# Kernel tuning notes

Measured on AMD Instinct MI355X. Metric: run time of the kernel, lower is better.

Reference implementation:

```python
import jax, jax.numpy as jnp
import numpy as np

N = 100000      # total nodes
E = 1600000     # total edges
B = 256         # graphs in batch
D_IN = 64       # node_in_dim
D_EMB = 128     # node_emb_dim
D_G = 128       # graph_emb_dim
L = 3           # gnn_layers
H1, H2 = 32, 8  # decoder MLP hidden dims
EPS_LN = 1e-5


def layernorm(h, g, b):
    mu = jnp.mean(h, -1, keepdims=True)
    var = jnp.mean((h - mu) ** 2, -1, keepdims=True)
    return (h - mu) * jax.lax.rsqrt(var + EPS_LN) * g + b


def setup_inputs() -> dict:
    key = jax.random.key(0)
    ks = jax.random.split(key, 16)
    gi = D_IN + D_EMB  # skip-conn GNN input dim

    def w(k, shape, fan):
        return jax.random.normal(k, shape, jnp.float32) / np.sqrt(fan).astype(np.float32)

    return {
        "x": jax.random.normal(ks[0], (N, D_IN), jnp.float32),
        "edge_index": jax.random.randint(ks[1], (2, E), 0, N),
        "batch_indices": jnp.sort(jax.random.randint(ks[2], (N,), 0, B)),
        "W_in": w(ks[3], (D_IN, D_EMB), D_IN), "b_in": jnp.zeros((D_EMB,), jnp.float32),
        "eps": jnp.zeros((L,), jnp.float32),  # GINConv train_eps init 0
        "mlp_W1": w(ks[4], (L, gi, D_EMB), gi), "mlp_b1": jnp.zeros((L, D_EMB), jnp.float32),
        "mlp_W2": w(ks[5], (L, D_EMB, D_EMB), D_EMB), "mlp_b2": jnp.zeros((L, D_EMB), jnp.float32),
        "ln_g": jnp.ones((L, D_EMB), jnp.float32), "ln_b": jnp.zeros((L, D_EMB), jnp.float32),
        "out_W": w(ks[6], (D_EMB, D_EMB), D_EMB), "out_b": jnp.zeros((D_EMB,), jnp.float32),
        "lnf_g": jnp.ones((D_EMB,), jnp.float32), "lnf_b": jnp.zeros((D_EMB,), jnp.float32),
        "graph_W": w(ks[7], (D_EMB, D_G), D_EMB), "graph_b": jnp.zeros((D_G,), jnp.float32),
        "gln_g": jnp.ones((D_G,), jnp.float32), "gln_b": jnp.zeros((D_G,), jnp.float32),
        "dW1": w(ks[8], (D_IN + D_EMB, H1), D_IN + D_EMB), "db1": jnp.zeros((H1,), jnp.float32),
        "dW2": w(ks[9], (H1, H2), H1), "db2": jnp.zeros((H2,), jnp.float32),
        "dW3": w(ks[10], (H2, 1), H2), "db3": jnp.zeros((1,), jnp.float32),
        "gW1": w(ks[11], (D_G, H1), D_G), "gb1": jnp.zeros((H1,), jnp.float32),
        "gW2": w(ks[12], (H1, H2), H1), "gb2": jnp.zeros((H2,), jnp.float32),
        "gW3": w(ks[13], (H2, 1), H2), "gb3": jnp.zeros((1,), jnp.float32),
    }


def reference(x, edge_index, batch_indices, W_in, b_in, eps, mlp_W1, mlp_b1, mlp_W2, mlp_b2,
              ln_g, ln_b, out_W, out_b, lnf_g, lnf_b, graph_W, graph_b, gln_g, gln_b,
              dW1, db1, dW2, db2, dW3, db3, gW1, gb1, gW2, gb2, gW3, gb3):
    src, dst = edge_index[0], edge_index[1]
    # Encoder: node_in_fc
    h = jax.nn.relu(x @ W_in + b_in)
    for l in range(L):
        gin = jnp.concatenate([x, h], -1)  # skip_conn: [N, D_IN+D_EMB]
        # GIN message passing: sum-aggregate neighbor features at target nodes
        agg = jax.ops.segment_sum(gin[src], dst, num_segments=N)
        z = (1.0 + eps[l]) * gin + agg
        z = jax.nn.relu(z @ mlp_W1[l] + mlp_b1[l]) @ mlp_W2[l] + mlp_b2[l]
        h = jax.nn.elu(layernorm(z, ln_g[l], ln_b[l]))
    # graph embedding: per-node fc+LN then global mean pool over batch segments
    ge = layernorm(jax.nn.relu(h @ graph_W + graph_b), gln_g, gln_b)
    sums = jax.ops.segment_sum(ge, batch_indices, num_segments=B)
    cnt = jax.ops.segment_sum(jnp.ones((N,), ge.dtype), batch_indices, num_segments=B)
    graph_emb = sums / jnp.maximum(cnt, 1.0)[:, None]
    # node_out_fc + final LN
    node_emb = layernorm(jax.nn.relu(h @ out_W + out_b), lnf_g, lnf_b)
    # Decoder: nodewise MLP on [x, node_emb] (skip_conn)
    ni = jnp.concatenate([x, node_emb], -1)
    no = jax.nn.relu(ni @ dW1 + db1)
    no = (jax.nn.relu(no @ dW2 + db2) @ dW3 + db3)[:, 0]  # [N]
    # graphwise residual MLP
    go = jax.nn.relu(graph_emb @ gW1 + gb1)
    go = (jax.nn.relu(go @ gW2 + gb2) @ gW3 + gb3)[:, 0]  # [B]
    return jnp.concatenate([no, go], -1)  # [N+B]
```

## Files before the change

kernel.cpp:

```cpp
#include <hip/hip_runtime.h>
#include <hip/hip_bf16.h>

#define D_IN 64
#define D_EMB 128
#define GI 192
#define H1 32
#define H2 8

typedef __attribute__((ext_vector_type(8))) short bf16x8;
typedef __attribute__((ext_vector_type(4))) float f32x4;

__device__ __forceinline__ unsigned short f2bf(float f) {
    unsigned int u = __float_as_uint(f);
    return (unsigned short)((u + 0x7fffu + ((u >> 16) & 1u)) >> 16);
}
__device__ __forceinline__ float bflo(unsigned int u) { return __uint_as_float(u << 16); }
__device__ __forceinline__ float bfhi(unsigned int u) { return __uint_as_float(u & 0xffff0000u); }
__device__ __forceinline__ unsigned int pk2(unsigned short a, unsigned short b) {
    return (unsigned int)a | ((unsigned int)b << 16);
}

__global__ __launch_bounds__(256) void hist_part_k(const int* __restrict__ dst, int* __restrict__ cnt,
                                                   int E, int N8) {
    int p = blockIdx.x & 7;
// ... 57 lines not shown
    }
}

__global__ __launch_bounds__(256) void scatter_part_k(const int* __restrict__ src, const int* __restrict__ dst,
                                                      int* __restrict__ cursor, int* __restrict__ csr,
                                                      int E, int N8) {
    int p = blockIdx.x & 7;
    int base = (blockIdx.x >> 3) * 1024;
    int lo = p * N8, hi = lo + N8;
    #pragma unroll
    for (int t = 0; t < 4; ++t) {
        int e = base + t * 256 + threadIdx.x;
        if (e < E) {
            int d = dst[e];
            if (d >= lo && d < hi) {
                int s = src[e];
                int pos = atomicAdd(&cursor[d], 1);
                csr[pos] = s;
            }
        }
    }
}

__global__ __launch_bounds__(256) void xcvt_k(const float* __restrict__ x, unsigned short* __restrict__ xb,
                                              int total4) {
    int i = blockIdx.x * 256 + threadIdx.x;
    if (i < total4) {
        float4 v = ((const float4*)x)[i];
        ((uint2*)xb)[i] = make_uint2(pk2(f2bf(v.x), f2bf(v.y)), pk2(f2bf(v.z), f2bf(v.w)));
    }
}

__global__ __launch_bounds__(256) void wfrag_all_k(
    const float* __restrict__ W_in, const float* __restrict__ mlp_W1, const float* __restrict__ mlp_W2,
    const float* __restrict__ graph_W, const float* __restrict__ out_W,
    unsigned short* __restrict__ wf_in, unsigned short* __restrict__ wf_w1,
    unsigned short* __restrict__ wf_w2, unsigned short* __restrict__ wf_graph,
    unsigned short* __restrict__ wf_out) {
    int idx = blockIdx.x * 256 + threadIdx.x;
    const float* src;
    unsigned short* dst;
    int local;
    if (idx < 8192) { src = W_in; dst = wf_in; local = idx; }
    else if (idx < 81920) { int t = idx - 8192; int l = t / 24576; local = t - l * 24576;
                            src = mlp_W1 + (size_t)l * 24576; dst = wf_w1 + (size_t)l * 24576; }
    else if (idx < 131072) { int t = idx - 81920; int l = t / 16384; local = t - l * 16384;
                             src = mlp_W2 + (size_t)l * 16384; dst = wf_w2 + (size_t)l * 16384; }
    else if (idx < 147456) { local = idx - 131072; src = graph_W; dst = wf_graph; }
    else { local = idx - 147456; src = out_W; dst = wf_out; }
    int k = local >> 7, c = local & 127;
    dst[(((size_t)(k >> 3) * 128) + c) * 8 + (k & 7)] = f2bf(src[local]);
}

__global__ __launch_bounds__(256) void agg64b_k(const unsigned short* __restrict__ xb,
                                                const int* __restrict__ rp, const int* __restrict__ cs,
                                                float* __restrict__ out, int N) {
    int n = blockIdx.x * 8 + (threadIdx.x >> 5);
    int lane = threadIdx.x & 31;
    if (n >= N) return;
    int bg = rp[n], e = rp[n + 1];
    const unsigned int* x2 = (const unsigned int*)xb;
    float sx = 0.f, sy = 0.f;
    int j = bg;
    for (; j + 3 < e; j += 4) {
        unsigned int v0 = x2[(size_t)cs[j] * 32 + lane];
        unsigned int v1 = x2[(size_t)cs[j + 1] * 32 + lane];
        unsigned int v2 = x2[(size_t)cs[j + 2] * 32 + lane];
        unsigned int v3 = x2[(size_t)cs[j + 3] * 32 + lane];
        sx += bflo(v0) + bflo(v1) + bflo(v2) + bflo(v3);
        sy += bfhi(v0) + bfhi(v1) + bfhi(v2) + bfhi(v3);
    }
    for (; j < e; ++j) {
        unsigned int v = x2[(size_t)cs[j] * 32 + lane];
        sx += bflo(v);
        sy += bfhi(v);
    }
    ((float2*)out)[(size_t)n * 32 + lane] = make_float2(sx, sy);
}

__global__ __launch_bounds__(256) void agg128b_k(const unsigned short* __restrict__ hb,
                                                 const int* __restrict__ rp, const int* __restrict__ cs,
                                                 float* __restrict__ out, int N) {
    int w = threadIdx.x >> 6, lane = threadIdx.x & 63;
    int n = blockIdx.x * 4 + w;
    if (n >= N) return;
    int bg = rp[n], e = rp[n + 1];
    const unsigned int* h2 = (const unsigned int*)hb;
    float sx = 0.f, sy = 0.f;
    int j = bg;
    for (; j + 3 < e; j += 4) {
        unsigned int v0 = h2[(size_t)cs[j] * 64 + lane];
        unsigned int v1 = h2[(size_t)cs[j + 1] * 64 + lane];
        unsigned int v2 = h2[(size_t)cs[j + 2] * 64 + lane];
        unsigned int v3 = h2[(size_t)cs[j + 3] * 64 + lane];
        sx += bflo(v0) + bflo(v1) + bflo(v2) + bflo(v3);
        sy += bfhi(v0) + bfhi(v1) + bfhi(v2) + bfhi(v3);
    }
    for (; j < e; ++j) {
        unsigned int v = h2[(size_t)cs[j] * 64 + lane];
        sx += bflo(v);
        sy += bfhi(v);
    }
    ((float2*)out)[(size_t)n * 64 + lane] = make_float2(sx, sy);
}

template <int RELU, int ELU>
__device__ __forceinline__ void ln_epilogue(
    f32x4 (&acc)[4][4], const float* __restrict__ bias,
    const float* __restrict__ g, const float* __restrict__ b,
    unsigned short* __restrict__ out,
    int rowBase, int wr, int wc, int lg, int l15, int wh,
    float* rsum, float* rsq, int N) {
    float bv[4], gv[4], bbv[4];
    #pragma unroll
    for (int cb = 0; cb < 4; ++cb) {
        int col = wc + cb * 16 + l15;
        bv[cb] = bias[col];
        gv[cb] = g[col];
        bbv[cb] = b[col];
    }
    float ps[4][4], pq[4][4];
    #pragma unroll
    for (int rb = 0; rb < 4; ++rb)
        #pragma unroll
        for (int q = 0; q < 4; ++q) {
            float s = 0.f, sq = 0.f;
            #pragma unroll
            for (int cb = 0; cb < 4; ++cb) {
                float v = acc[rb][cb][q] + bv[cb];
                if (RELU) v = fmaxf(v, 0.f);
                s += v;
                sq += v * v;
            }
            ps[rb][q] = s;
            pq[rb][q] = sq;
        }
    #pragma unroll
    for (int m = 1; m < 16; m <<= 1) {
        #pragma unroll
        for (int rb = 0; rb < 4; ++rb)
            #pragma unroll
            for (int q = 0; q < 4; ++q) {
                ps[rb][q] += __shfl_xor(ps[rb][q], m, 64);
                pq[rb][q] += __shfl_xor(pq[rb][q], m, 64);
            }
    }
    if (l15 == 0) {
        #pragma unroll
        for (int rb = 0; rb < 4; ++rb)
            #pragma unroll
            for (int q = 0; q < 4; ++q) {
                int row = wr + rb * 16 + lg * 4 + q;
                rsum[wh * 128 + row] = ps[rb][q];
                rsq[wh * 128 + row] = pq[rb][q];
            }
    }
    __syncthreads();
    #pragma unroll
// ... 26 lines not shown
    __shared__ unsigned short As[4 * 128 * 8];
    const int tid = threadIdx.x;
    const int wid = tid >> 6, lane = tid & 63;
    const int l15 = lane & 15, lg = lane >> 4;
    const int rowBase = blockIdx.x * 128;
    const int wr = (wid >> 1) * 64, wc = (wid & 1) * 64;
    f32x4 zero = {0.f, 0.f, 0.f, 0.f};
    f32x4 acc[4][4];
    #pragma unroll
    for (int i = 0; i < 4; ++i)
        #pragma unroll
        for (int j = 0; j < 4; ++j) acc[i][j] = zero;
    const int r = tid >> 1, hp = tid & 1;
    const int arow = min(rowBase + r, N - 1);

    for (int k0 = 0; k0 < D_IN; k0 += 32) {
        bf16x8 bfr[4];
        const int G = (k0 >> 3) + lg;
        #pragma unroll
        for (int cb = 0; cb < 4; ++cb)
            bfr[cb] = *(const bf16x8*)&Wf[(((size_t)G * 128) + wc + cb * 16 + l15) * 8];
        __syncthreads();
        #pragma unroll
        for (int g2 = 0; g2 < 2; ++g2) {
            int gg = hp * 2 + g2;
            int k = k0 + gg * 8;
            uint4 w = *(const uint4*)(Abf + (size_t)arow * D_IN + k);
            *(uint4*)&As[(((size_t)gg * 128) + r) * 8] = w;
        }
        __syncthreads();
        #pragma unroll
        for (int rb = 0; rb < 4; ++rb) {
            bf16x8 afr = *(const bf16x8*)&As[(((size_t)lg * 128) + wr + rb * 16 + l15) * 8];
            #pragma unroll
            for (int cb = 0; cb < 4; ++cb)
                acc[rb][cb] = __builtin_amdgcn_mfma_f32_16x16x32_bf16(afr, bfr[cb], acc[rb][cb], 0, 0, 0);
        }
    }
    #pragma unroll
    for (int cb = 0; cb < 4; ++cb) {
        int col = wc + cb * 16 + l15;
        float bvv = bias[col];
        #pragma unroll
        for (int rb = 0; rb < 4; ++rb)
            #pragma unroll
            for (int q = 0; q < 4; ++q) {
                int row = rowBase + wr + rb * 16 + lg * 4 + q;
                if (row < N) C[(size_t)row * D_EMB + col] = f2bf(fmaxf(acc[rb][cb][q] + bvv, 0.f));
            }
    }
}

__global__ __launch_bounds__(256) void gin_layer_k(
    const unsigned short* __restrict__ xb, const unsigned short* __restrict__ hbi,
    const float* __restrict__ aggx, const float* __restrict__ aggh, const float* __restrict__ epsp,
    const unsigned short* __restrict__ W1f, const float* __restrict__ b1,
    const unsigned short* __restrict__ W2f, const float* __restrict__ b2,
    const float* __restrict__ lng, const float* __restrict__ lnb,
    unsigned short* __restrict__ hbo, int N) {
    __shared__ unsigned short As[4 * 128 * 8];
    __shared__ unsigned short T1[16 * 128 * 8];
    __shared__ float rsum[2 * 128];
    __shared__ float rsq[2 * 128];

    const int tid = threadIdx.x;
    const int wid = tid >> 6, lane = tid & 63;
    const int l15 = lane & 15, lg = lane >> 4;
    const int rowBase = blockIdx.x * 128;
    const int wr = (wid >> 1) * 64, wc = (wid & 1) * 64;
    const int wh = wid & 1;

    f32x4 zero = {0.f, 0.f, 0.f, 0.f};
    f32x4 acc[4][4];
    #pragma unroll
    for (int i = 0; i < 4; ++i)
        #pragma unroll
        for (int j = 0; j < 4; ++j) acc[i][j] = zero;

    const float es = 1.0f + epsp[0];
    const int r = tid >> 1, hp = tid & 1;
    const int arow = min(rowBase + r, N - 1);

    for (int k0 = 0; k0 < GI; k0 += 32) {
        bf16x8 bfr[4];
        const int G = (k0 >> 3) + lg;
        #pragma unroll
        for (int cb = 0; cb < 4; ++cb)
            bfr[cb] = *(const bf16x8*)&W1f[(((size_t)G * 128) + wc + cb * 16 + l15) * 8];
        __syncthreads();
        #pragma unroll
        for (int g2 = 0; g2 < 2; ++g2) {
            int gg = hp * 2 + g2;
            int k = k0 + gg * 8;
            float f[8], ga[8];
            if (k < D_IN) {
                uint4 xv = *(const uint4*)(xb + (size_t)arow * D_IN + k);
                const float* gp = aggx + (size_t)arow * D_IN + k;
                float4 g0 = *(const float4*)gp, g1 = *(const float4*)(gp + 4);
                f[0] = bflo(xv.x); f[1] = bfhi(xv.x); f[2] = bflo(xv.y); f[3] = bfhi(xv.y);
                f[4] = bflo(xv.z); f[5] = bfhi(xv.z); f[6] = bflo(xv.w); f[7] = bfhi(xv.w);
                ga[0] = g0.x; ga[1] = g0.y; ga[2] = g0.z; ga[3] = g0.w;
                ga[4] = g1.x; ga[5] = g1.y; ga[6] = g1.z; ga[7] = g1.w;
            } else {
                int kk = k - D_IN;
                uint4 hv = *(const uint4*)(hbi + (size_t)arow * D_EMB + kk);
                const float* gp = aggh + (size_t)arow * D_EMB + kk;
                float4 g0 = *(const float4*)gp, g1 = *(const float4*)(gp + 4);
                f[0] = bflo(hv.x); f[1] = bfhi(hv.x); f[2] = bflo(hv.y); f[3] = bfhi(hv.y);
                f[4] = bflo(hv.z); f[5] = bfhi(hv.z); f[6] = bflo(hv.w); f[7] = bfhi(hv.w);
                ga[0] = g0.x; ga[1] = g0.y; ga[2] = g0.z; ga[3] = g0.w;
                ga[4] = g1.x; ga[5] = g1.y; ga[6] = g1.z; ga[7] = g1.w;
            }
            unsigned short o[8];
            #pragma unroll
            for (int i = 0; i < 8; ++i) o[i] = f2bf(fmaf(es, f[i], ga[i]));
            *(uint4*)&As[(((size_t)gg * 128) + r) * 8] =
                make_uint4(pk2(o[0], o[1]), pk2(o[2], o[3]), pk2(o[4], o[5]), pk2(o[6], o[7]));
        }
        __syncthreads();
        #pragma unroll
        for (int rb = 0; rb < 4; ++rb) {
            bf16x8 afr = *(const bf16x8*)&As[(((size_t)lg * 128) + wr + rb * 16 + l15) * 8];
            #pragma unroll
            for (int cb = 0; cb < 4; ++cb)
                acc[rb][cb] = __builtin_amdgcn_mfma_f32_16x16x32_bf16(afr, bfr[cb], acc[rb][cb], 0, 0, 0);
        }
    }

    #pragma unroll
    for (int cb = 0; cb < 4; ++cb) {
        int col = wc + cb * 16 + l15;
        float bvv = b1[col];
        #pragma unroll
        for (int rb = 0; rb < 4; ++rb)
            #pragma unroll
            for (int q = 0; q < 4; ++q) {
                int row = wr + rb * 16 + lg * 4 + q;
                float v = fmaxf(acc[rb][cb][q] + bvv, 0.f);
                T1[(((size_t)(col >> 3) * 128) + row) * 8 + (col & 7)] = f2bf(v);
            }
    }
    __syncthreads();

    f32x4 acc2[4][4];
    #pragma unroll
    for (int i = 0; i < 4; ++i)
        #pragma unroll
        for (int j = 0; j < 4; ++j) acc2[i][j] = zero;
    for (int k0 = 0; k0 < D_EMB; k0 += 32) {
        bf16x8 bfr[4];
        const int G = (k0 >> 3) + lg;
        #pragma unroll
        for (int cb = 0; cb < 4; ++cb)
            bfr[cb] = *(const bf16x8*)&W2f[(((size_t)G * 128) + wc + cb * 16 + l15) * 8];
        #pragma unroll
        for (int rb = 0; rb < 4; ++rb) {
            bf16x8 afr = *(const bf16x8*)&T1[(((size_t)G * 128) + wr + rb * 16 + l15) * 8];
            #pragma unroll
            for (int cb = 0; cb < 4; ++cb)
                acc2[rb][cb] = __builtin_amdgcn_mfma_f32_16x16x32_bf16(afr, bfr[cb], acc2[rb][cb], 0, 0, 0);
        }
    }

    ln_epilogue<0, 1>(acc2, b2, lng, lnb, hbo, rowBase, wr, wc, lg, l15, wh, rsum, rsq, N);
}

template <int RELU, int ELU>
__global__ __launch_bounds__(256) void fc_ln_k(
    const unsigned short* __restrict__ Abf, const unsigned short* __restrict__ Wf,
    const float* __restrict__ bias, const float* __restrict__ g, const float* __restrict__ b,
    unsigned short* __restrict__ out, int N) {
    __shared__ unsigned short As[4 * 128 * 8];
    __shared__ float rsum[2 * 128];
    __shared__ float rsq[2 * 128];
    const int tid = threadIdx.x;
    const int wid = tid >> 6, lane = tid & 63;
    const int l15 = lane & 15, lg = lane >> 4;
    const int rowBase = blockIdx.x * 128;
    const int wr = (wid >> 1) * 64, wc = (wid & 1) * 64;
    const int wh = wid & 1;
    f32x4 zero = {0.f, 0.f, 0.f, 0.f};
    f32x4 acc[4][4];
    #pragma unroll
    for (int i = 0; i < 4; ++i)
        #pragma unroll
        for (int j = 0; j < 4; ++j) acc[i][j] = zero;
    const int r = tid >> 1, hp = tid & 1;
    const int arow = min(rowBase + r, N - 1);

    for (int k0 = 0; k0 < D_EMB; k0 += 32) {
        bf16x8 bfr[4];
        const int G = (k0 >> 3) + lg;
        #pragma unroll
        for (int cb = 0; cb < 4; ++cb)
            bfr[cb] = *(const bf16x8*)&Wf[(((size_t)G * 128) + wc + cb * 16 + l15) * 8];
        __syncthreads();
        #pragma unroll
        for (int g2 = 0; g2 < 2; ++g2) {
            int gg = hp * 2 + g2;
            int k = k0 + gg * 8;
            uint4 w = *(const uint4*)(Abf + (size_t)arow * D_EMB + k);
            *(uint4*)&As[(((size_t)gg * 128) + r) * 8] = w;
        }
        __syncthreads();
        #pragma unroll
        for (int rb = 0; rb < 4; ++rb) {
            bf16x8 afr = *(const bf16x8*)&As[(((size_t)lg * 128) + wr + rb * 16 + l15) * 8];
            #pragma unroll
            for (int cb = 0; cb < 4; ++cb)
                acc[rb][cb] = __builtin_amdgcn_mfma_f32_16x16x32_bf16(afr, bfr[cb], acc[rb][cb], 0, 0, 0);
        }
    }
    ln_epilogue<RELU, ELU>(acc, bias, g, b, out, rowBase, wr, wc, lg, l15, wh, rsum, rsq, N);
}

__global__ __launch_bounds__(256) void bounds_k(const int* __restrict__ batch, int* __restrict__ bounds,
                                                int N, int B) {
    int i = blockIdx.x * 256 + threadIdx.x;
    if (i <= B) {
        int lo = 0, hi = N;
        while (lo < hi) { int m = (lo + hi) >> 1; if (batch[m] < i) lo = m + 1; else hi = m; }
        bounds[i] = lo;
    }
}

__global__ __launch_bounds__(128) void pool_part_k(const unsigned short* __restrict__ ge,
                                                   const int* __restrict__ bounds,
                                                   float* __restrict__ gemb) {
    int b = blockIdx.x >> 3;
    int s = blockIdx.x & 7;
    int start = bounds[b], end = bounds[b + 1];
    int len = end - start;
    int c0 = start + (int)(((long long)len * s) >> 3);
    int c1 = start + (int)(((long long)len * (s + 1)) >> 3);
    if (c1 <= c0) return;
    int col = threadIdx.x;
    float sum = 0.f;
    for (int n = c0; n < c1; ++n)
        sum += __uint_as_float((unsigned int)ge[(size_t)n * D_EMB + col] << 16);
    atomicAdd(&gemb[(size_t)b * D_EMB + col], sum);
}

__global__ __launch_bounds__(256) void node_dec_k(
    const float* __restrict__ x, const unsigned short* __restrict__ ne,
    const float* __restrict__ W1, const float* __restrict__ b1,
    const float* __restrict__ W2, const float* __restrict__ b2,
    const float* __restrict__ W3, const float* __restrict__ b3,
    float* __restrict__ out, int N) {
    __shared__ float W1s[GI * H1];
    __shared__ float W2s[H1 * H2];
    __shared__ float W3s[H2];
    __shared__ float b1s[H1], b2s[H2];
    for (int i = threadIdx.x; i < GI * H1; i += 256) W1s[i] = W1[i];
    if (threadIdx.x < H1 * H2) W2s[threadIdx.x] = W2[threadIdx.x];
    if (threadIdx.x < H2) { W3s[threadIdx.x] = W3[threadIdx.x]; b2s[threadIdx.x] = b2[threadIdx.x]; }
    if (threadIdx.x < H1) b1s[threadIdx.x] = b1[threadIdx.x];
    __syncthreads();
    int n = blockIdx.x * 256 + threadIdx.x;
    if (n >= N) return;
    float acc[H1];
    #pragma unroll
    for (int j = 0; j < H1; ++j) acc[j] = b1s[j];
    const float4* xr = (const float4*)(x + (size_t)n * D_IN);
    #pragma unroll 4
    for (int q = 0; q < D_IN / 4; ++q) {
        float4 v = xr[q];
// ... 84 lines not shown
    #pragma unroll
    for (int m = 0; m < H2; ++m) o = fmaf(fmaxf(a2[m], 0.f), W3s[m], o);
    out[gidx] = o;
}

extern "C" void kernel_launch(void* const* d_in, const int* in_sizes, int n_in,
                              void* d_out, int out_size, void* d_ws, size_t ws_size,
                              hipStream_t stream) {
    const float* x       = (const float*)d_in[0];
    const int*   ei      = (const int*)d_in[1];
    const int*   batch   = (const int*)d_in[2];
    const float* W_in    = (const float*)d_in[3];
    const float* b_in    = (const float*)d_in[4];
    const float* eps     = (const float*)d_in[5];
    const float* mlp_W1  = (const float*)d_in[6];
    const float* mlp_b1  = (const float*)d_in[7];
    const float* mlp_W2  = (const float*)d_in[8];
    const float* mlp_b2  = (const float*)d_in[9];
    const float* ln_g    = (const float*)d_in[10];
    const float* ln_b    = (const float*)d_in[11];
    const float* out_W   = (const float*)d_in[12];
    const float* out_b   = (const float*)d_in[13];
    const float* lnf_g   = (const float*)d_in[14];
    const float* lnf_b   = (const float*)d_in[15];
    const float* graph_W = (const float*)d_in[16];
    const float* graph_b = (const float*)d_in[17];
    const float* gln_g   = (const float*)d_in[18];
    const float* gln_b   = (const float*)d_in[19];
    const float* dW1     = (const float*)d_in[20];
    const float* db1     = (const float*)d_in[21];
    const float* dW2     = (const float*)d_in[22];
    const float* db2     = (const float*)d_in[23];
    const float* dW3     = (const float*)d_in[24];
    const float* db3     = (const float*)d_in[25];
    const float* gW1     = (const float*)d_in[26];
    const float* gb1     = (const float*)d_in[27];
    const float* gW2     = (const float*)d_in[28];
    const float* gb2     = (const float*)d_in[29];
    const float* gW3     = (const float*)d_in[30];
    const float* gb3     = (const float*)d_in[31];
    float* out = (float*)d_out;

    const int N = in_sizes[0] / D_IN;
    const int E = in_sizes[1] / 2;
    const int B = out_size - N;
    const int N8 = (N + 7) / 8;

    const int* esrc = ei;
    const int* edst = ei + E;

    size_t off = 0;
    auto alloc = [&](size_t bytes) { size_t o = off; off += (bytes + 255) & ~(size_t)255; return o; };
    char* ws = (char*)d_ws;
    unsigned short* xb  = (unsigned short*)(ws + alloc((size_t)N * D_IN * 2));
    unsigned short* hb0 = (unsigned short*)(ws + alloc((size_t)N * D_EMB * 2));
    unsigned short* hb1 = (unsigned short*)(ws + alloc((size_t)N * D_EMB * 2));
    float* aggx = (float*)(ws + alloc((size_t)N * D_IN * 4));
    float* aggh = (float*)(ws + alloc((size_t)N * D_EMB * 4));
    float* gemb = (float*)(ws + alloc((size_t)B * D_EMB * 4));
    unsigned short* wfpool = (unsigned short*)(ws + alloc((size_t)163840 * 2));
    int* row_ptr = (int*)(ws + alloc((size_t)(N + 1) * 4));
    int* cnt     = (int*)(ws + alloc((size_t)N * 4));
    int* bsum    = (int*)(ws + alloc(512 * 4));
    int* bounds  = (int*)(ws + alloc((size_t)(B + 1) * 4));
    int* csr     = (int*)(ws + alloc((size_t)E * 4));
    (void)ws_size;

    unsigned short* wf_in    = wfpool;
    unsigned short* wf_w1    = wf_in + (size_t)64 * 128;
    unsigned short* wf_w2    = wf_w1 + (size_t)3 * 192 * 128;
    unsigned short* wf_graph = wf_w2 + (size_t)3 * 128 * 128;
    unsigned short* wf_out   = wf_graph + (size_t)128 * 128;

    unsigned short* zb  = hb0;
    unsigned short* neb = (unsigned short*)aggh;

    const int NB = (N + 255) / 256;
    const int gridEP = 8 * ((E + 1023) / 1024);
    const int gridN4 = (N + 3) / 4;
    const int gridG = (N + 127) / 128;

    hipMemsetAsync(cnt, 0, (size_t)N * 4, stream);
    hist_part_k<<<gridEP, 256, 0, stream>>>(edst, cnt, E, N8);
    scan1_k<<<NB, 256, 0, stream>>>(cnt, row_ptr, bsum, N);
    scan2_k<<<1, 512, 0, stream>>>(bsum, NB);
    scan3_k<<<(N + 256) / 256, 256, 0, stream>>>(row_ptr, bsum, cnt, N, E);
    scatter_part_k<<<gridEP, 256, 0, stream>>>(esrc, edst, cnt, csr, E, N8);

    xcvt_k<<<(N * D_IN / 4 + 255) / 256, 256, 0, stream>>>(x, xb, N * D_IN / 4);
    wfrag_all_k<<<640, 256, 0, stream>>>(W_in, mlp_W1, mlp_W2, graph_W, out_W,
                                         wf_in, wf_w1, wf_w2, wf_graph, wf_out);
    bounds_k<<<(B + 256) / 256, 256, 0, stream>>>(batch, bounds, N, B);
    hipMemsetAsync(gemb, 0, (size_t)B * D_EMB * 4, stream);

    agg64b_k<<<(N + 7) / 8, 256, 0, stream>>>(xb, row_ptr, csr, aggx, N);

    enc_gemm_k<<<gridG, 256, 0, stream>>>(xb, wf_in, b_in, hb0, N);

    unsigned short* hin = hb0;
    unsigned short* hout = hb1;
    for (int l = 0; l < 3; ++l) {
        agg128b_k<<<gridN4, 256, 0, stream>>>(hin, row_ptr, csr, aggh, N);
        gin_layer_k<<<gridG, 256, 0, stream>>>(xb, hin, aggx, aggh, eps + l,
                                               wf_w1 + (size_t)l * 192 * 128, mlp_b1 + (size_t)l * D_EMB,
                                               wf_w2 + (size_t)l * 128 * 128, mlp_b2 + (size_t)l * D_EMB,
                                               ln_g + (size_t)l * D_EMB, ln_b + (size_t)l * D_EMB,
                                               hout, N);
        unsigned short* t = hin; hin = hout; hout = t;
    }

    fc_ln_k<1, 0><<<gridG, 256, 0, stream>>>(hin, wf_graph, graph_b, gln_g, gln_b, zb, N);
    pool_part_k<<<B * 8, 128, 0, stream>>>(zb, bounds, gemb);

    fc_ln_k<1, 0><<<gridG, 256, 0, stream>>>(hin, wf_out, out_b, lnf_g, lnf_b, neb, N);

    node_dec_k<<<(N + 255) / 256, 256, 0, stream>>>(x, neb, dW1, db1, dW2, db2, dW3, db3, out, N);
    graph_dec_k<<<1, 256, 0, stream>>>(gemb, bounds, gW1, gb1, gW2, gb2, gW3, gb3, out + N, B);
}
```

Measured before the change: 828.5 us.

## Split neighbor aggregation into column blocks with edge-parallel lane groups

Replaces the two per-node gather kernels with one templated kernel. Each block now handles a 16-column (64-byte) slice of the feature row for 16 nodes. Within a wavefront, four lane groups each take every fourth edge and their partial sums are combined with cross-lane shuffles. The aim is more memory-level parallelism per wavefront, and column blocking may keep gathered slices resident in cache across blocks that handle the same columns. In exchange, each wavefront issues 64-byte segments instead of full-row coalesced reads, the CSR index array is read once per column block, and shuffle reductions are added.

New measurement: 1.096 ms. +32.3%, slower.

```diff
diff --git a/kernel.cpp b/kernel.cpp
--- a/kernel.cpp
+++ b/kernel.cpp
@@ -133,56 +133,40 @@
     dst[(((size_t)(k >> 3) * 128) + c) * 8 + (k & 7)] = f2bf(src[local]);
 }
 
-__global__ __launch_bounds__(256) void agg64b_k(const unsigned short* __restrict__ xb,
-                                                const int* __restrict__ rp, const int* __restrict__ cs,
-                                                float* __restrict__ out, int N) {
-    int n = blockIdx.x * 8 + (threadIdx.x >> 5);
-    int lane = threadIdx.x & 31;
-    if (n >= N) return;
-    int bg = rp[n], e = rp[n + 1];
-    const unsigned int* x2 = (const unsigned int*)xb;
-    float sx = 0.f, sy = 0.f;
-    int j = bg;
-    for (; j + 3 < e; j += 4) {
-        unsigned int v0 = x2[(size_t)cs[j] * 32 + lane];
-        unsigned int v1 = x2[(size_t)cs[j + 1] * 32 + lane];
-        unsigned int v2 = x2[(size_t)cs[j + 2] * 32 + lane];
-        unsigned int v3 = x2[(size_t)cs[j + 3] * 32 + lane];
-        sx += bflo(v0) + bflo(v1) + bflo(v2) + bflo(v3);
-        sy += bfhi(v0) + bfhi(v1) + bfhi(v2) + bfhi(v3);
-    }
-    for (; j < e; ++j) {
-        unsigned int v = x2[(size_t)cs[j] * 32 + lane];
-        sx += bflo(v);
-        sy += bfhi(v);
-    }
-    ((float2*)out)[(size_t)n * 32 + lane] = make_float2(sx, sy);
-}
-
-__global__ __launch_bounds__(256) void agg128b_k(const unsigned short* __restrict__ hb,
+template <int ROW_UINTS, int NCB>
+__global__ __launch_bounds__(256) void agg_col_k(const unsigned short* __restrict__ tb,
                                                  const int* __restrict__ rp, const int* __restrict__ cs,
                                                  float* __restrict__ out, int N) {
-    int w = threadIdx.x >> 6, lane = threadIdx.x & 63;
-    int n = blockIdx.x * 4 + w;
-    if (n >= N) return;
-    int bg = rp[n], e = rp[n + 1];
-    const unsigned int* h2 = (const unsigned int*)hb;
-    float sx = 0.f, sy = 0.f;
-    int j = bg;
-    for (; j + 3 < e; j += 4) {
-        unsigned int v0 = h2[(size_t)cs[j] * 64 + lane];
-        unsigned int v1 = h2[(size_t)cs[j + 1] * 64 + lane];
-        unsigned int v2 = h2[(size_t)cs[j + 2] * 64 + lane];
-        unsigned int v3 = h2[(size_t)cs[j + 3] * 64 + lane];
-        sx += bflo(v0) + bflo(v1) + bflo(v2) + bflo(v3);
-        sy += bfhi(v0) + bfhi(v1) + bfhi(v2) + bfhi(v3);
-    }
-    for (; j < e; ++j) {
-        unsigned int v = h2[(size_t)cs[j] * 64 + lane];
-        sx += bflo(v);
-        sy += bfhi(v);
-    }
-    ((float2*)out)[(size_t)n * 64 + lane] = make_float2(sx, sy);
+    const int cb = blockIdx.x & (NCB - 1);
+    const int rowchunk = blockIdx.x / NCB;
+    const int wid = threadIdx.x >> 6, lane = threadIdx.x & 63;
+    const int l15 = lane & 15, lg = lane >> 4;
+    const unsigned int* t2 = (const unsigned int*)tb;
+    const int basec = cb * 16 + l15;
+
+    #pragma unroll
+    for (int i = 0; i < 4; ++i) {
+        int n = rowchunk * 16 + wid * 4 + i;
+        if (n >= N) return;
+        int bg = rp[n], en = rp[n + 1];
+        float sx = 0.f, sy = 0.f;
+        int j = bg + lg;
+        for (; j + 4 < en; j += 8) {
+            unsigned int v0 = t2[(size_t)cs[j] * ROW_UINTS + basec];
+            unsigned int v1 = t2[(size_t)cs[j + 4] * ROW_UINTS + basec];
+            sx += bflo(v0) + bflo(v1);
+            sy += bfhi(v0) + bfhi(v1);
+        }
+        if (j < en) {
+            unsigned int v = t2[(size_t)cs[j] * ROW_UINTS + basec];
+            sx += bflo(v);
+            sy += bfhi(v);
+        }
+        sx += __shfl_xor(sx, 16, 64); sx += __shfl_xor(sx, 32, 64);
+        sy += __shfl_xor(sy, 16, 64); sy += __shfl_xor(sy, 32, 64);
+        if (lg == 0)
+            ((float2*)out)[(size_t)n * ROW_UINTS + basec] = make_float2(sx, sy);
+    }
 }
 
 template <int RELU, int ELU>
@@ -692,8 +676,8 @@
 
     const int NB = (N + 255) / 256;
     const int gridEP = 8 * ((E + 1023) / 1024);
-    const int gridN4 = (N + 3) / 4;
     const int gridG = (N + 127) / 128;
+    const int gridA = (N + 15) / 16;
 
     hipMemsetAsync(cnt, 0, (size_t)N * 4, stream);
     hist_part_k<<<gridEP, 256, 0, stream>>>(edst, cnt, E, N8);
@@ -708,14 +692,14 @@
     bounds_k<<<(B + 256) / 256, 256, 0, stream>>>(batch, bounds, N, B);
     hipMemsetAsync(gemb, 0, (size_t)B * D_EMB * 4, stream);
 
-    agg64b_k<<<(N + 7) / 8, 256, 0, stream>>>(xb, row_ptr, csr, aggx, N);
+    agg_col_k<32, 2><<<2 * gridA, 256, 0, stream>>>(xb, row_ptr, csr, aggx, N);
 
     enc_gemm_k<<<gridG, 256, 0, stream>>>(xb, wf_in, b_in, hb0, N);
 
     unsigned short* hin = hb0;
     unsigned short* hout = hb1;
     for (int l = 0; l < 3; ++l) {
-        agg128b_k<<<gridN4, 256, 0, stream>>>(hin, row_ptr, csr, aggh, N);
+        agg_col_k<64, 4><<<4 * gridA, 256, 0, stream>>>(hin, row_ptr, csr, aggh, N);
         gin_layer_k<<<gridG, 256, 0, stream>>>(xb, hin, aggx, aggh, eps + l,
                                                wf_w1 + (size_t)l * 192 * 128, mlp_b1 + (size_t)l * D_EMB,
                                                wf_w2 + (size_t)l * 128 * 128, mlp_b2 + (size_t)l * D_EMB,
```

## Fuse 128-wide neighbor aggregation into GIN layer kernel via shared-memory tile

Applied to the files above, without the earlier changes.

Removes the separate agg128b kernel and its fp32 aggh buffer. Each gin_layer block now gathers neighbor rows for its 128 nodes itself, with one wave handling 32 rows. It adds (1+eps)*h and writes the bf16 result into a shared tile that feeds the W1 MFMA for the hidden part of K, and that tile is then reused for the intermediate activation. This drops the fp32 aggregate write and read round trip and one launch per layer. The cost is that the gather now runs serially inside the GEMM kernel, with only 782 blocks and little parallelism per wave, so latency hiding may get worse.

After: 1.308 ms. 57.9% more time.

```diff
diff --git a/kernel.cpp b/kernel.cpp
--- a/kernel.cpp
+++ b/kernel.cpp
@@ -159,32 +159,6 @@
     ((float2*)out)[(size_t)n * 32 + lane] = make_float2(sx, sy);
 }
 
-__global__ __launch_bounds__(256) void agg128b_k(const unsigned short* __restrict__ hb,
-                                                 const int* __restrict__ rp, const int* __restrict__ cs,
-                                                 float* __restrict__ out, int N) {
-    int w = threadIdx.x >> 6, lane = threadIdx.x & 63;
-    int n = blockIdx.x * 4 + w;
-    if (n >= N) return;
-    int bg = rp[n], e = rp[n + 1];
-    const unsigned int* h2 = (const unsigned int*)hb;
-    float sx = 0.f, sy = 0.f;
-    int j = bg;
-    for (; j + 3 < e; j += 4) {
-        unsigned int v0 = h2[(size_t)cs[j] * 64 + lane];
-        unsigned int v1 = h2[(size_t)cs[j + 1] * 64 + lane];
-        unsigned int v2 = h2[(size_t)cs[j + 2] * 64 + lane];
-        unsigned int v3 = h2[(size_t)cs[j + 3] * 64 + lane];
-        sx += bflo(v0) + bflo(v1) + bflo(v2) + bflo(v3);
-        sy += bfhi(v0) + bfhi(v1) + bfhi(v2) + bfhi(v3);
-    }
-    for (; j < e; ++j) {
-        unsigned int v = h2[(size_t)cs[j] * 64 + lane];
-        sx += bflo(v);
-        sy += bfhi(v);
-    }
-    ((float2*)out)[(size_t)n * 64 + lane] = make_float2(sx, sy);
-}
-
 template <int RELU, int ELU>
 __device__ __forceinline__ void ln_epilogue(
     f32x4 (&acc)[4][4], const float* __restrict__ bias,
@@ -318,13 +292,14 @@
 
 __global__ __launch_bounds__(256) void gin_layer_k(
     const unsigned short* __restrict__ xb, const unsigned short* __restrict__ hbi,
-    const float* __restrict__ aggx, const float* __restrict__ aggh, const float* __restrict__ epsp,
+    const float* __restrict__ aggx, const float* __restrict__ epsp,
+    const int* __restrict__ rp, const int* __restrict__ cs,
     const unsigned short* __restrict__ W1f, const float* __restrict__ b1,
     const unsigned short* __restrict__ W2f, const float* __restrict__ b2,
     const float* __restrict__ lng, const float* __restrict__ lnb,
     unsigned short* __restrict__ hbo, int N) {
+    __shared__ unsigned short ZT[16 * 128 * 8];
     __shared__ unsigned short As[4 * 128 * 8];
-    __shared__ unsigned short T1[16 * 128 * 8];
     __shared__ float rsum[2 * 128];
     __shared__ float rsq[2 * 128];
 
@@ -334,6 +309,40 @@
     const int rowBase = blockIdx.x * 128;
     const int wr = (wid >> 1) * 64, wc = (wid & 1) * 64;
     const int wh = wid & 1;
+    const float es = 1.0f + epsp[0];
+
+    {
+        const unsigned int* h2 = (const unsigned int*)hbi;
+        const int zg = lane >> 2;
+        const int ze = (2 * lane) & 7;
+        for (int i = 0; i < 32; ++i) {
+            int row = wid * 32 + i;
+            int n = rowBase + row;
+            float sx = 0.f, sy = 0.f;
+            if (n < N) {
+                int bg = rp[n], en = rp[n + 1];
+                int j = bg;
+                for (; j + 3 < en; j += 4) {
+                    unsigned int v0 = h2[(size_t)cs[j] * 64 + lane];
+                    unsigned int v1 = h2[(size_t)cs[j + 1] * 64 + lane];
+                    unsigned int v2 = h2[(size_t)cs[j + 2] * 64 + lane];
+                    unsigned int v3 = h2[(size_t)cs[j + 3] * 64 + lane];
+                    sx += bflo(v0) + bflo(v1) + bflo(v2) + bflo(v3);
+                    sy += bfhi(v0) + bfhi(v1) + bfhi(v2) + bfhi(v3);
+                }
+                for (; j < en; ++j) {
+                    unsigned int v = h2[(size_t)cs[j] * 64 + lane];
+                    sx += bflo(v);
+                    sy += bfhi(v);
+                }
+                unsigned int hv = h2[(size_t)n * 64 + lane];
+                sx = fmaf(es, bflo(hv), sx);
+                sy = fmaf(es, bfhi(hv), sy);
+            }
+            *(unsigned int*)&ZT[(((size_t)zg * 128) + row) * 8 + ze] = pk2(f2bf(sx), f2bf(sy));
+        }
+    }
+    __syncthreads();
 
     f32x4 zero = {0.f, 0.f, 0.f, 0.f};
     f32x4 acc[4][4];
@@ -342,11 +351,10 @@
         #pragma unroll
         for (int j = 0; j < 4; ++j) acc[i][j] = zero;
 
-    const float es = 1.0f + epsp[0];
     const int r = tid >> 1, hp = tid & 1;
     const int arow = min(rowBase + r, N - 1);
 
-    for (int k0 = 0; k0 < GI; k0 += 32) {
+    for (int k0 = 0; k0 < D_IN; k0 += 32) {
         bf16x8 bfr[4];
         const int G = (k0 >> 3) + lg;
         #pragma unroll
@@ -357,28 +365,18 @@
         for (int g2 = 0; g2 < 2; ++g2) {
             int gg = hp * 2 + g2;
             int k = k0 + gg * 8;
-            float f[8], ga[8];
-            if (k < D_IN) {
-                uint4 xv = *(const uint4*)(xb + (size_t)arow * D_IN + k);
-                const float* gp = aggx + (size_t)arow * D_IN + k;
-                float4 g0 = *(const float4*)gp, g1 = *(const float4*)(gp + 4);
-                f[0] = bflo(xv.x); f[1] = bfhi(xv.x); f[2] = bflo(xv.y); f[3] = bfhi(xv.y);
-                f[4] = bflo(xv.z); f[5] = bfhi(xv.z); f[6] = bflo(xv.w); f[7] = bfhi(xv.w);
-                ga[0] = g0.x; ga[1] = g0.y; ga[2] = g0.z; ga[3] = g0.w;
-                ga[4] = g1.x; ga[5] = g1.y; ga[6] = g1.z; ga[7] = g1.w;
-            } else {
-                int kk = k - D_IN;
-                uint4 hv = *(const uint4*)(hbi + (size_t)arow * D_EMB + kk);
-                const float* gp = aggh + (size_t)arow * D_EMB + kk;
-                float4 g0 = *(const float4*)gp, g1 = *(const float4*)(gp + 4);
-                f[0] = bflo(hv.x); f[1] = bfhi(hv.x); f[2] = bflo(hv.y); f[3] = bfhi(hv.y);
-                f[4] = bflo(hv.z); f[5] = bfhi(hv.z); f[6] = bflo(hv.w); f[7] = bfhi(hv.w);
-                ga[0] = g0.x; ga[1] = g0.y; ga[2] = g0.z; ga[3] = g0.w;
-                ga[4] = g1.x; ga[5] = g1.y; ga[6] = g1.z; ga[7] = g1.w;
-            }
+            uint4 xv = *(const uint4*)(xb + (size_t)arow * D_IN + k);
+            const float* gp = aggx + (size_t)arow * D_IN + k;
+            float4 g0 = *(const float4*)gp, g1 = *(const float4*)(gp + 4);
             unsigned short o[8];
-            #pragma unroll
-            for (int i = 0; i < 8; ++i) o[i] = f2bf(fmaf(es, f[i], ga[i]));
+            o[0] = f2bf(fmaf(es, bflo(xv.x), g0.x));
+            o[1] = f2bf(fmaf(es, bfhi(xv.x), g0.y));
+            o[2] = f2bf(fmaf(es, bflo(xv.y), g0.z));
+            o[3] = f2bf(fmaf(es, bfhi(xv.y), g0.w));
+            o[4] = f2bf(fmaf(es, bflo(xv.z), g1.x));
+            o[5] = f2bf(fmaf(es, bfhi(xv.z), g1.y));
+            o[6] = f2bf(fmaf(es, bflo(xv.w), g1.z));
+            o[7] = f2bf(fmaf(es, bfhi(xv.w), g1.w));
             *(uint4*)&As[(((size_t)gg * 128) + r) * 8] =
                 make_uint4(pk2(o[0], o[1]), pk2(o[2], o[3]), pk2(o[4], o[5]), pk2(o[6], o[7]));
         }
@@ -391,7 +389,23 @@
                 acc[rb][cb] = __builtin_amdgcn_mfma_f32_16x16x32_bf16(afr, bfr[cb], acc[rb][cb], 0, 0, 0);
         }
     }
-
+    for (int k0 = D_IN; k0 < GI; k0 += 32) {
+        bf16x8 bfr[4];
+        const int G = (k0 >> 3) + lg;
+        const int ZG = ((k0 - D_IN) >> 3) + lg;
+        #pragma unroll
+        for (int cb = 0; cb < 4; ++cb)
+            bfr[cb] = *(const bf16x8*)&W1f[(((size_t)G * 128) + wc + cb * 16 + l15) * 8];
+        #pragma unroll
+        for (int rb = 0; rb < 4; ++rb) {
+            bf16x8 afr = *(const bf16x8*)&ZT[(((size_t)ZG * 128) + wr + rb * 16 + l15) * 8];
+            #pragma unroll
+            for (int cb = 0; cb < 4; ++cb)
+                acc[rb][cb] = __builtin_amdgcn_mfma_f32_16x16x32_bf16(afr, bfr[cb], acc[rb][cb], 0, 0, 0);
+        }
+    }
+
+    __syncthreads();
     #pragma unroll
     for (int cb = 0; cb < 4; ++cb) {
         int col = wc + cb * 16 + l15;
@@ -402,7 +416,7 @@
             for (int q = 0; q < 4; ++q) {
                 int row = wr + rb * 16 + lg * 4 + q;
                 float v = fmaxf(acc[rb][cb][q] + bvv, 0.f);
-                T1[(((size_t)(col >> 3) * 128) + row) * 8 + (col & 7)] = f2bf(v);
+                ZT[(((size_t)(col >> 3) * 128) + row) * 8 + (col & 7)] = f2bf(v);
             }
     }
     __syncthreads();
@@ -420,7 +434,7 @@
             bfr[cb] = *(const bf16x8*)&W2f[(((size_t)G * 128) + wc + cb * 16 + l15) * 8];
         #pragma unroll
         for (int rb = 0; rb < 4; ++rb) {
-            bf16x8 afr = *(const bf16x8*)&T1[(((size_t)G * 128) + wr + rb * 16 + l15) * 8];
+            bf16x8 afr = *(const bf16x8*)&ZT[(((size_t)G * 128) + wr + rb * 16 + l15) * 8];
             #pragma unroll
             for (int cb = 0; cb < 4; ++cb)
                 acc2[rb][cb] = __builtin_amdgcn_mfma_f32_16x16x32_bf16(afr, bfr[cb], acc2[rb][cb], 0, 0, 0);
@@ -671,7 +685,6 @@
     unsigned short* hb0 = (unsigned short*)(ws + alloc((size_t)N * D_EMB * 2));
     unsigned short* hb1 = (unsigned short*)(ws + alloc((size_t)N * D_EMB * 2));
     float* aggx = (float*)(ws + alloc((size_t)N * D_IN * 4));
-    float* aggh = (float*)(ws + alloc((size_t)N * D_EMB * 4));
     float* gemb = (float*)(ws + alloc((size_t)B * D_EMB * 4));
     unsigned short* wfpool = (unsigned short*)(ws + alloc((size_t)163840 * 2));
     int* row_ptr = (int*)(ws + alloc((size_t)(N + 1) * 4));
@@ -688,11 +701,10 @@
     unsigned short* wf_out   = wf_graph + (size_t)128 * 128;
 
     unsigned short* zb  = hb0;
-    unsigned short* neb = (unsigned short*)aggh;
+    unsigned short* neb = (unsigned short*)aggx;
 
     const int NB = (N + 255) / 256;
     const int gridEP = 8 * ((E + 1023) / 1024);
-    const int gridN4 = (N + 3) / 4;
     const int gridG = (N + 127) / 128;
 
     hipMemsetAsync(cnt, 0, (size_t)N * 4, stream);
@@ -715,8 +727,7 @@
     unsigned short* hin = hb0;
     unsigned short* hout = hb1;
     for (int l = 0; l < 3; ++l) {
-        agg128b_k<<<gridN4, 256, 0, stream>>>(hin, row_ptr, csr, aggh, N);
-        gin_layer_k<<<gridG, 256, 0, stream>>>(xb, hin, aggx, aggh, eps + l,
+        gin_layer_k<<<gridG, 256, 0, stream>>>(xb, hin, aggx, eps + l, row_ptr, csr,
                                                wf_w1 + (size_t)l * 192 * 128, mlp_b1 + (size_t)l * D_EMB,
                                                wf_w2 + (size_t)l * 128 * 128, mlp_b2 + (size_t)l * D_EMB,
                                                ln_g + (size_t)l * D_EMB, ln_b + (size_t)l * D_EMB,
```

## Fuse GIN self-term into aggregation, store aggregates as bf16, merge final FC kernels

Applied to the files above, without the earlier changes.

The neighbor aggregation kernel now adds the (1+eps)*h self term and writes a bf16 z tensor, so the GIN layer loads z directly instead of reading both h and an fp32 aggregate. The x aggregate is also stored in bf16. The two per-node FC+LayerNorm kernels (graph and node output) become one kernel that shares the A tile loads and runs two accumulator sets. The intent is to cut HBM traffic and one kernel launch, at the cost of extra bf16 rounding of the aggregates and higher register pressure in the merged FC kernel.

Measured after the change: 819.9 us. Within noise of the previous version (-1.0%).

```diff
diff --git a/kernel.cpp b/kernel.cpp
--- a/kernel.cpp
+++ b/kernel.cpp
@@ -135,7 +135,7 @@
 
 __global__ __launch_bounds__(256) void agg64b_k(const unsigned short* __restrict__ xb,
                                                 const int* __restrict__ rp, const int* __restrict__ cs,
-                                                float* __restrict__ out, int N) {
+                                                unsigned short* __restrict__ outb, int N) {
     int n = blockIdx.x * 8 + (threadIdx.x >> 5);
     int lane = threadIdx.x & 31;
     if (n >= N) return;
@@ -156,15 +156,17 @@
         sx += bflo(v);
         sy += bfhi(v);
     }
-    ((float2*)out)[(size_t)n * 32 + lane] = make_float2(sx, sy);
-}
-
-__global__ __launch_bounds__(256) void agg128b_k(const unsigned short* __restrict__ hb,
-                                                 const int* __restrict__ rp, const int* __restrict__ cs,
-                                                 float* __restrict__ out, int N) {
+    ((unsigned int*)outb)[(size_t)n * 32 + lane] = pk2(f2bf(sx), f2bf(sy));
+}
+
+__global__ __launch_bounds__(256) void aggz_k(const unsigned short* __restrict__ hb,
+                                              const int* __restrict__ rp, const int* __restrict__ cs,
+                                              const float* __restrict__ epsp,
+                                              unsigned short* __restrict__ zh, int N) {
     int w = threadIdx.x >> 6, lane = threadIdx.x & 63;
     int n = blockIdx.x * 4 + w;
     if (n >= N) return;
+    float es = 1.0f + epsp[0];
     int bg = rp[n], e = rp[n + 1];
     const unsigned int* h2 = (const unsigned int*)hb;
     float sx = 0.f, sy = 0.f;
@@ -182,7 +184,10 @@
         sx += bflo(v);
         sy += bfhi(v);
     }
-    ((float2*)out)[(size_t)n * 64 + lane] = make_float2(sx, sy);
+    unsigned int hv = h2[(size_t)n * 64 + lane];
+    sx = fmaf(es, bflo(hv), sx);
+    sy = fmaf(es, bfhi(hv), sy);
+    ((unsigned int*)zh)[(size_t)n * 64 + lane] = pk2(f2bf(sx), f2bf(sy));
 }
 
 template <int RELU, int ELU>
@@ -317,8 +322,8 @@
 }
 
 __global__ __launch_bounds__(256) void gin_layer_k(
-    const unsigned short* __restrict__ xb, const unsigned short* __restrict__ hbi,
-    const float* __restrict__ aggx, const float* __restrict__ aggh, const float* __restrict__ epsp,
+    const unsigned short* __restrict__ xb, const unsigned short* __restrict__ aggxb,
+    const unsigned short* __restrict__ zhb, const float* __restrict__ epsp,
     const unsigned short* __restrict__ W1f, const float* __restrict__ b1,
     const unsigned short* __restrict__ W2f, const float* __restrict__ b2,
     const float* __restrict__ lng, const float* __restrict__ lnb,
@@ -357,30 +362,24 @@
         for (int g2 = 0; g2 < 2; ++g2) {
             int gg = hp * 2 + g2;
             int k = k0 + gg * 8;
-            float f[8], ga[8];
+            uint4 w;
             if (k < D_IN) {
                 uint4 xv = *(const uint4*)(xb + (size_t)arow * D_IN + k);
-                const float* gp = aggx + (size_t)arow * D_IN + k;
-                float4 g0 = *(const float4*)gp, g1 = *(const float4*)(gp + 4);
-                f[0] = bflo(xv.x); f[1] = bfhi(xv.x); f[2] = bflo(xv.y); f[3] = bfhi(xv.y);
-                f[4] = bflo(xv.z); f[5] = bfhi(xv.z); f[6] = bflo(xv.w); f[7] = bfhi(xv.w);
-                ga[0] = g0.x; ga[1] = g0.y; ga[2] = g0.z; ga[3] = g0.w;
-                ga[4] = g1.x; ga[5] = g1.y; ga[6] = g1.z; ga[7] = g1.w;
+                uint4 av = *(const uint4*)(aggxb + (size_t)arow * D_IN + k);
+                unsigned short o[8];
+                o[0] = f2bf(fmaf(es, bflo(xv.x), bflo(av.x)));
+                o[1] = f2bf(fmaf(es, bfhi(xv.x), bfhi(av.x)));
+                o[2] = f2bf(fmaf(es, bflo(xv.y), bflo(av.y)));
+                o[3] = f2bf(fmaf(es, bfhi(xv.y), bfhi(av.y)));
+                o[4] = f2bf(fmaf(es, bflo(xv.z), bflo(av.z)));
+                o[5] = f2bf(fmaf(es, bfhi(xv.z), bfhi(av.z)));
+                o[6] = f2bf(fmaf(es, bflo(xv.w), bflo(av.w)));
+                o[7] = f2bf(fmaf(es, bfhi(xv.w), bfhi(av.w)));
+                w = make_uint4(pk2(o[0], o[1]), pk2(o[2], o[3]), pk2(o[4], o[5]), pk2(o[6], o[7]));
             } else {
-                int kk = k - D_IN;
-                uint4 hv = *(const uint4*)(hbi + (size_t)arow * D_EMB + kk);
-                const float* gp = aggh + (size_t)arow * D_EMB + kk;
-                float4 g0 = *(const float4*)gp, g1 = *(const float4*)(gp + 4);
-                f[0] = bflo(hv.x); f[1] = bfhi(hv.x); f[2] = bflo(hv.y); f[3] = bfhi(hv.y);
-                f[4] = bflo(hv.z); f[5] = bfhi(hv.z); f[6] = bflo(hv.w); f[7] = bfhi(hv.w);
-                ga[0] = g0.x; ga[1] = g0.y; ga[2] = g0.z; ga[3] = g0.w;
-                ga[4] = g1.x; ga[5] = g1.y; ga[6] = g1.z; ga[7] = g1.w;
-            }
-            unsigned short o[8];
-            #pragma unroll
-            for (int i = 0; i < 8; ++i) o[i] = f2bf(fmaf(es, f[i], ga[i]));
-            *(uint4*)&As[(((size_t)gg * 128) + r) * 8] =
-                make_uint4(pk2(o[0], o[1]), pk2(o[2], o[3]), pk2(o[4], o[5]), pk2(o[6], o[7]));
+                w = *(const uint4*)(zhb + (size_t)arow * D_EMB + (k - D_IN));
+            }
+            *(uint4*)&As[(((size_t)gg * 128) + r) * 8] = w;
         }
         __syncthreads();
         #pragma unroll
@@ -430,11 +429,13 @@
     ln_epilogue<0, 1>(acc2, b2, lng, lnb, hbo, rowBase, wr, wc, lg, l15, wh, rsum, rsq, N);
 }
 
-template <int RELU, int ELU>
-__global__ __launch_bounds__(256) void fc_ln_k(
-    const unsigned short* __restrict__ Abf, const unsigned short* __restrict__ Wf,
-    const float* __restrict__ bias, const float* __restrict__ g, const float* __restrict__ b,
-    unsigned short* __restrict__ out, int N) {
+__global__ __launch_bounds__(256) void fc2_k(
+    const unsigned short* __restrict__ Abf,
+    const unsigned short* __restrict__ WfG, const float* __restrict__ biasG,
+    const float* __restrict__ gG, const float* __restrict__ bG, unsigned short* __restrict__ outG,
+    const unsigned short* __restrict__ WfN, const float* __restrict__ biasN,
+    const float* __restrict__ gN, const float* __restrict__ bN, unsigned short* __restrict__ outN,
+    int N) {
     __shared__ unsigned short As[4 * 128 * 8];
     __shared__ float rsum[2 * 128];
     __shared__ float rsq[2 * 128];
@@ -445,20 +446,22 @@
     const int wr = (wid >> 1) * 64, wc = (wid & 1) * 64;
     const int wh = wid & 1;
     f32x4 zero = {0.f, 0.f, 0.f, 0.f};
-    f32x4 acc[4][4];
+    f32x4 accG[4][4], accN[4][4];
     #pragma unroll
     for (int i = 0; i < 4; ++i)
         #pragma unroll
-        for (int j = 0; j < 4; ++j) acc[i][j] = zero;
+        for (int j = 0; j < 4; ++j) { accG[i][j] = zero; accN[i][j] = zero; }
     const int r = tid >> 1, hp = tid & 1;
     const int arow = min(rowBase + r, N - 1);
 
     for (int k0 = 0; k0 < D_EMB; k0 += 32) {
-        bf16x8 bfr[4];
+        bf16x8 bfrG[4], bfrN[4];
         const int G = (k0 >> 3) + lg;
         #pragma unroll
-        for (int cb = 0; cb < 4; ++cb)
-            bfr[cb] = *(const bf16x8*)&Wf[(((size_t)G * 128) + wc + cb * 16 + l15) * 8];
+        for (int cb = 0; cb < 4; ++cb) {
+            bfrG[cb] = *(const bf16x8*)&WfG[(((size_t)G * 128) + wc + cb * 16 + l15) * 8];
+            bfrN[cb] = *(const bf16x8*)&WfN[(((size_t)G * 128) + wc + cb * 16 + l15) * 8];
+        }
         __syncthreads();
         #pragma unroll
         for (int g2 = 0; g2 < 2; ++g2) {
@@ -472,11 +475,15 @@
         for (int rb = 0; rb < 4; ++rb) {
             bf16x8 afr = *(const bf16x8*)&As[(((size_t)lg * 128) + wr + rb * 16 + l15) * 8];
             #pragma unroll
-            for (int cb = 0; cb < 4; ++cb)
-                acc[rb][cb] = __builtin_amdgcn_mfma_f32_16x16x32_bf16(afr, bfr[cb], acc[rb][cb], 0, 0, 0);
-        }
-    }
-    ln_epilogue<RELU, ELU>(acc, bias, g, b, out, rowBase, wr, wc, lg, l15, wh, rsum, rsq, N);
+            for (int cb = 0; cb < 4; ++cb) {
+                accG[rb][cb] = __builtin_amdgcn_mfma_f32_16x16x32_bf16(afr, bfrG[cb], accG[rb][cb], 0, 0, 0);
+                accN[rb][cb] = __builtin_amdgcn_mfma_f32_16x16x32_bf16(afr, bfrN[cb], accN[rb][cb], 0, 0, 0);
+            }
+        }
+    }
+    ln_epilogue<1, 0>(accG, biasG, gG, bG, outG, rowBase, wr, wc, lg, l15, wh, rsum, rsq, N);
+    __syncthreads();
+    ln_epilogue<1, 0>(accN, biasN, gN, bN, outN, rowBase, wr, wc, lg, l15, wh, rsum, rsq, N);
 }
 
 __global__ __launch_bounds__(256) void bounds_k(const int* __restrict__ batch, int* __restrict__ bounds,
@@ -667,11 +674,11 @@
     size_t off = 0;
     auto alloc = [&](size_t bytes) { size_t o = off; off += (bytes + 255) & ~(size_t)255; return o; };
     char* ws = (char*)d_ws;
-    unsigned short* xb  = (unsigned short*)(ws + alloc((size_t)N * D_IN * 2));
-    unsigned short* hb0 = (unsigned short*)(ws + alloc((size_t)N * D_EMB * 2));
-    unsigned short* hb1 = (unsigned short*)(ws + alloc((size_t)N * D_EMB * 2));
-    float* aggx = (float*)(ws + alloc((size_t)N * D_IN * 4));
-    float* aggh = (float*)(ws + alloc((size_t)N * D_EMB * 4));
+    unsigned short* xb    = (unsigned short*)(ws + alloc((size_t)N * D_IN * 2));
+    unsigned short* hb0   = (unsigned short*)(ws + alloc((size_t)N * D_EMB * 2));
+    unsigned short* hb1   = (unsigned short*)(ws + alloc((size_t)N * D_EMB * 2));
+    unsigned short* zh    = (unsigned short*)(ws + alloc((size_t)N * D_EMB * 2));
+    unsigned short* aggxb = (unsigned short*)(ws + alloc((size_t)N * D_IN * 2));
     float* gemb = (float*)(ws + alloc((size_t)B * D_EMB * 4));
     unsigned short* wfpool = (unsigned short*)(ws + alloc((size_t)163840 * 2));
     int* row_ptr = (int*)(ws + alloc((size_t)(N + 1) * 4));
@@ -687,9 +694,6 @@
     unsigned short* wf_graph = wf_w2 + (size_t)3 * 128 * 128;
     unsigned short* wf_out   = wf_graph + (size_t)128 * 128;
 
-    unsigned short* zb  = hb0;
-    unsigned short* neb = (unsigned short*)aggh;
-
     const int NB = (N + 255) / 256;
     const int gridEP = 8 * ((E + 1023) / 1024);
     const int gridN4 = (N + 3) / 4;
@@ -708,26 +712,28 @@
     bounds_k<<<(B + 256) / 256, 256, 0, stream>>>(batch, bounds, N, B);
     hipMemsetAsync(gemb, 0, (size_t)B * D_EMB * 4, stream);
 
-    agg64b_k<<<(N + 7) / 8, 256, 0, stream>>>(xb, row_ptr, csr, aggx, N);
+    agg64b_k<<<(N + 7) / 8, 256, 0, stream>>>(xb, row_ptr, csr, aggxb, N);
 
     enc_gemm_k<<<gridG, 256, 0, stream>>>(xb, wf_in, b_in, hb0, N);
 
     unsigned short* hin = hb0;
     unsigned short* hout = hb1;
     for (int l = 0; l < 3; ++l) {
-        agg128b_k<<<gridN4, 256, 0, stream>>>(hin, row_ptr, csr, aggh, N);
-        gin_layer_k<<<gridG, 256, 0, stream>>>(xb, hin, aggx, aggh, eps + l,
+        aggz_k<<<gridN4, 256, 0, stream>>>(hin, row_ptr, csr, eps + l, zh, N);
+        gin_layer_k<<<gridG, 256, 0, stream>>>(xb, aggxb, zh, eps + l,
                                                wf_w1 + (size_t)l * 192 * 128, mlp_b1 + (size_t)l * D_EMB,
                                                wf_w2 + (size_t)l * 128 * 128, mlp_b2 + (size_t)l * D_EMB,
                                                ln_g + (size_t)l * D_EMB, ln_b + (size_t)l * D_EMB,
                                                hout, N);
         unsigned short* t = hin; hin = hout; hout = t;
     }
-
-    fc_ln_k<1, 0><<<gridG, 256, 0, stream>>>(hin, wf_graph, graph_b, gln_g, gln_b, zb, N);
+    unsigned short* zb  = hb0;
+    unsigned short* neb = zh;
+
+    fc2_k<<<gridG, 256, 0, stream>>>(hin,
+                                     wf_graph, graph_b, gln_g, gln_b, zb,
+                                     wf_out, out_b, lnf_g, lnf_b, neb, N);
     pool_part_k<<<B * 8, 128, 0, stream>>>(zb, bounds, gemb);
-
-    fc_ln_k<1, 0><<<gridG, 256, 0, stream>>>(hin, wf_out, out_b, lnf_g, lnf_b, neb, N);
 
     node_dec_k<<<(N + 255) / 256, 256, 0, stream>>>(x, neb, dW1, db1, dW2, db2, dW3, db3, out, N);
     graph_dec_k<<<1, 256, 0, stream>>>(gemb, bounds, gW1, gb1, gW2, gb2, gW3, gb3, out + N, B);
```
